# Kernel optimization log

Measured on AMD Instinct MI355X. Metric: run time of the kernel, lower is better.

The kernel has to match this reference:

```python
import jax, jax.numpy as jnp
import numpy as np

H = 128
EPS = 1e-5
INFERENCE_BIAS = 0.1


def setup_inputs() -> dict:
    key = jax.random.key(0)
    ks = jax.random.split(key, 10)
    n_users, n_foods, E = 100000, 50000, 1000000
    z_user = jax.random.normal(ks[0], (n_users, H), dtype=jnp.float32)
    z_food = jax.random.normal(ks[1], (n_foods, H), dtype=jnp.float32)
    row = jax.random.randint(ks[2], (E,), 0, n_users, dtype=jnp.int64)
    col = jax.random.randint(ks[3], (E,), 0, n_foods, dtype=jnp.int64)
    # lin1: Linear(2H -> H); lin2: Linear(H -> 1)
    W1 = jax.random.normal(ks[4], (H, 2 * H), dtype=jnp.float32) * (1.0 / np.sqrt(2 * H))
    b1 = jnp.zeros((H,), dtype=jnp.float32)
    gamma = jnp.ones((H,), dtype=jnp.float32)
    beta = jnp.zeros((H,), dtype=jnp.float32)
    running_mean = jax.random.normal(ks[5], (H,), dtype=jnp.float32) * 0.1
    running_var = jnp.abs(jax.random.normal(ks[6], (H,), dtype=jnp.float32)) * 0.1 + 1.0
    W2 = jax.random.normal(ks[7], (1, H), dtype=jnp.float32) * (1.0 / np.sqrt(H))
    b2 = jnp.zeros((1,), dtype=jnp.float32)
    return {"z_user": z_user, "z_food": z_food, "row": row, "col": col,
            "W1": W1, "b1": b1, "gamma": gamma, "beta": beta,
            "running_mean": running_mean, "running_var": running_var,
            "W2": W2, "b2": b2}


def reference(z_user, z_food, row, col, W1, b1, gamma, beta,
              running_mean, running_var, W2, b2):
    # gather per-edge endpoint embeddings and concat: [E, 2H]
    z = jnp.concatenate([z_user[row], z_food[col]], axis=-1)
    h = z @ W1.T + b1                                        # [E, H]
    # BatchNorm1d in eval mode: running statistics
    h = (h - running_mean) * jax.lax.rsqrt(running_var + EPS) * gamma + beta
    h = jax.nn.relu(h)                                        # dropout is identity in eval
    out = h @ W2.T + b2                                       # [E, 1]
    return jax.nn.sigmoid((out + INFERENCE_BIAS).reshape(-1)) # [E]
```

## Files before the change

### kernel.cpp

```cpp
#include <hip/hip_runtime.h>
#include <hip/hip_bf16.h>
#include <math.h>

#define H 128
#define EPS 1e-5f
#define INF_BIAS 0.1f

typedef __attribute__((ext_vector_type(8))) short bf16x8;
typedef __attribute__((ext_vector_type(4))) float f32x4;

__device__ inline unsigned short f2bf_rne(float f) {
    unsigned u = __float_as_uint(f);
    u += 0x7fffu + ((u >> 16) & 1u);
    return (unsigned short)(u >> 16);
}
__device__ inline float bf2f(unsigned short h) {
    return __uint_as_float(((unsigned)h) << 16);
}
__device__ inline unsigned pack2(float a, float b) {
    return (unsigned)f2bf_rne(a) | ((unsigned)f2bf_rne(b) << 16);
}
__device__ inline float2 unpack2(unsigned v) {
    float2 r;
    r.x = __uint_as_float(v << 16);
    r.y = __uint_as_float(v & 0xffff0000u);
    return r;
}

__global__ void prep_kernel(
    const float* __restrict__ W1, const float* __restrict__ b1,
    const float* __restrict__ gamma, const float* __restrict__ beta,
    const float* __restrict__ rm, const float* __restrict__ rv,
    unsigned short* __restrict__ Wswz_u, unsigned short* __restrict__ Wswz_f,
    float* __restrict__ d_user)
{
    const int f    = blockIdx.x;
    const int half = f >> 4, nt = (f >> 2) & 3, kt = f & 3;
    const int t    = threadIdx.x;
    const int c    = t & 15, q = t >> 4;

    const int j  = half * 64 + (c >> 2) * 16 + nt * 4 + (c & 3);
    const float a = gamma[j] * rsqrtf(rv[j] + EPS);
    const int k0 = kt * 32 + q * 8;

    unsigned short wu[8], wf[8];
    #pragma unroll
    for (int i = 0; i < 8; ++i) {
        wu[i] = f2bf_rne(a * W1[(size_t)j * (2 * H) + k0 + i]);
        wf[i] = f2bf_rne(a * W1[(size_t)j * (2 * H) + H + k0 + i]);
    }
    const size_t dst = (size_t)f * 512 + (size_t)t * 8;
    #pragma unroll
    for (int i = 0; i < 8; ++i) { Wswz_u[dst + i] = wu[i]; Wswz_f[dst + i] = wf[i]; }

    if (kt == 0 && q == 0) d_user[j] = a * (b1[j] - rm[j]) + beta[j];
}

__global__ __launch_bounds__(256, 2) void proj_mfma(
    const float* __restrict__ z_user, const float* __restrict__ z_food,
    const unsigned short* __restrict__ Wswz_u, const unsigned short* __restrict__ Wswz_f,
    const float* __restrict__ d_user,
    unsigned short* __restrict__ U, unsigned short* __restrict__ F,
    int n_users, int n_foods, int GU, int GB)
{
    const bool userMode = (blockIdx.x < (unsigned)GU);
    const float* Z;
    const unsigned short* Wsrc;
    unsigned short* Out;
    int n, blk0, nblk;
    if (userMode) { Z = z_user; Wsrc = Wswz_u; Out = U; n = n_users; blk0 = blockIdx.x;      nblk = GU; }
    else          { Z = z_food; Wsrc = Wswz_f; Out = F; n = n_foods; blk0 = blockIdx.x - GU; nblk = GB - GU; }
    const int tiles = n >> 4;

    const int wave = threadIdx.x >> 6;
    const int lane = threadIdx.x & 63;
    const int c = lane & 15;
    const int q = lane >> 4;
    const int wg   = blk0 * 4 + wave;
    const int half = wg & 1;
    const int pair = wg >> 1;
    const int stride = nblk * 2;

    bf16x8 wf[4][4];
    #pragma unroll
    for (int nt = 0; nt < 4; ++nt)
        #pragma unroll
        for (int kt = 0; kt < 4; ++kt)
            wf[nt][kt] = *(const bf16x8*)(Wsrc + (size_t)(half * 16 + nt * 4 + kt) * 512 + lane * 8);

    f32x4 dvec[4];
    #pragma unroll
    for (int nt = 0; nt < 4; ++nt) {
        if (userMode) {
            float4 d = *(const float4*)(d_user + half * 64 + q * 16 + nt * 4);
            dvec[nt] = (f32x4){d.x, d.y, d.z, d.w};
        } else {
            dvec[nt] = (f32x4){0.f, 0.f, 0.f, 0.f};
        }
    }

    auto loadZ = [&](int t, float4 zb[8]) {
        const float* zrow = Z + (size_t)(min(t, tiles - 1) * 16 + c) * H;
        #pragma unroll
        for (int kt = 0; kt < 4; ++kt) {
            const int k0 = kt * 32 + q * 8;
            zb[2 * kt + 0] = ((const float4*)(zrow + k0))[0];
            zb[2 * kt + 1] = ((const float4*)(zrow + k0))[1];
        }
    };

    auto computeStore = [&](int t, const float4 zb[8]) {
        f32x4 acc[4];
        #pragma unroll
        for (int nt = 0; nt < 4; ++nt) acc[nt] = dvec[nt];

        #pragma unroll
        for (int kt = 0; kt < 4; ++kt) {
            float4 za = zb[2 * kt + 0];
            float4 zv = zb[2 * kt + 1];
            bf16x8 zhi, zlo;
            {
                float v[8] = {za.x, za.y, za.z, za.w, zv.x, zv.y, zv.z, zv.w};
                #pragma unroll
                for (int i = 0; i < 8; ++i) {
                    unsigned short hi = f2bf_rne(v[i]);
                    unsigned short lo = f2bf_rne(v[i] - bf2f(hi));
                    zhi[i] = (short)hi; zlo[i] = (short)lo;
                }
            }
            #pragma unroll
            for (int nt = 0; nt < 4; ++nt) {
                acc[nt] = __builtin_amdgcn_mfma_f32_16x16x32_bf16(wf[nt][kt], zhi, acc[nt], 0, 0, 0);
                acc[nt] = __builtin_amdgcn_mfma_f32_16x16x32_bf16(wf[nt][kt], zlo, acc[nt], 0, 0, 0);
            }
        }

        if (t < tiles) {
            const int r = t * 16 + c;
            unsigned short* obase = Out + (size_t)r * H + half * 64 + q * 16;
            uint4 p0, p1;
            p0.x = pack2(acc[0][0], acc[0][1]); p0.y = pack2(acc[0][2], acc[0][3]);
            p0.z = pack2(acc[1][0], acc[1][1]); p0.w = pack2(acc[1][2], acc[1][3]);
            p1.x = pack2(acc[2][0], acc[2][1]); p1.y = pack2(acc[2][2], acc[2][3]);
            p1.z = pack2(acc[3][0], acc[3][1]); p1.w = pack2(acc[3][2], acc[3][3]);
            *(uint4*)(obase)     = p0;
            *(uint4*)(obase + 8) = p1;
        }
    };

    int nIt = (tiles + stride - 1) / stride;
    nIt = (nIt + 1) & ~1;

    float4 zb0[8], zb1[8];
    int t = pair;
    loadZ(t, zb0);
    for (int it = 0; it < nIt; it += 2) {
        loadZ(t + stride, zb1);
        computeStore(t, zb0);
        if (it + 2 < nIt) loadZ(t + 2 * stride, zb0);
        computeStore(t + stride, zb1);
        t += 2 * stride;
    }
}

#define EUN 8
__global__ __launch_bounds__(256, 4) void edge_kernel(
    const unsigned short* __restrict__ U, const unsigned short* __restrict__ F,
    const int* __restrict__ row, const int* __restrict__ col,
    const float* __restrict__ W2, const float* __restrict__ b2,
    float* __restrict__ out, int E)
{
    const int lane = threadIdx.x & 15;
    const int g  = (blockIdx.x * blockDim.x + threadIdx.x) >> 4;
    const int nG = (gridDim.x * blockDim.x) >> 4;

    const float4 w2a = ((const float4*)W2)[2 * lane];
    const float4 w2b = ((const float4*)W2)[2 * lane + 1];
    const float bias = b2[0] + INF_BIAS;

    for (int e0 = g; e0 < E; e0 += EUN * nG) {
        int iu[EUN], ifo[EUN];
        #pragma unroll
        for (int i = 0; i < EUN; ++i) {
            int e  = e0 + i * nG;
            int ec = (e < E) ? e : e0;
            iu[i]  = row[ec];
            ifo[i] = col[ec];
        }
        uint4 uv[EUN], fv[EUN];
        #pragma unroll
        for (int i = 0; i < EUN; ++i) {
            uv[i] = ((const uint4*)(U + (size_t)iu[i]  * H))[lane];
            fv[i] = ((const uint4*)(F + (size_t)ifo[i] * H))[lane];
        }
        #pragma unroll
        for (int i = 0; i < EUN; ++i) {
            float2 u0 = unpack2(uv[i].x), f0 = unpack2(fv[i].x);
            float2 u1 = unpack2(uv[i].y), f1 = unpack2(fv[i].y);
            float2 u2 = unpack2(uv[i].z), f2 = unpack2(fv[i].z);
            float2 u3 = unpack2(uv[i].w), f3 = unpack2(fv[i].w);

            float s =
                w2a.x * fmaxf(u0.x + f0.x, 0.0f) +
                w2a.y * fmaxf(u0.y + f0.y, 0.0f) +
                w2a.z * fmaxf(u1.x + f1.x, 0.0f) +
                w2a.w * fmaxf(u1.y + f1.y, 0.0f) +
                w2b.x * fmaxf(u2.x + f2.x, 0.0f) +
                w2b.y * fmaxf(u2.y + f2.y, 0.0f) +
                w2b.z * fmaxf(u3.x + f3.x, 0.0f) +
                w2b.w * fmaxf(u3.y + f3.y, 0.0f);

            s += __shfl_xor(s, 8, 16);
            s += __shfl_xor(s, 4, 16);
            s += __shfl_xor(s, 2, 16);
            s += __shfl_xor(s, 1, 16);

            const int e = e0 + i * nG;
            if (lane == 0 && e < E) {
                float x = s + bias;
                out[e] = 1.0f / (1.0f + __expf(-x));
            }
        }
    }
}

extern "C" void kernel_launch(void* const* d_in, const int* in_sizes, int n_in,
                              void* d_out, int out_size, void* d_ws, size_t ws_size,
                              hipStream_t stream) {
    const float* z_user = (const float*)d_in[0];
    const float* z_food = (const float*)d_in[1];
    const int*   row    = (const int*)d_in[2];
    const int*   col    = (const int*)d_in[3];
    const float* W1     = (const float*)d_in[4];
    const float* b1     = (const float*)d_in[5];
    const float* gamma  = (const float*)d_in[6];
    const float* beta   = (const float*)d_in[7];
    const float* rm     = (const float*)d_in[8];
    const float* rv     = (const float*)d_in[9];
    const float* W2     = (const float*)d_in[10];
    const float* b2     = (const float*)d_in[11];
    float* out = (float*)d_out;

    const int n_users = in_sizes[0] / H;
    const int n_foods = in_sizes[1] / H;
    const int E       = in_sizes[2];

    unsigned short* U      = (unsigned short*)d_ws;
    unsigned short* F      = U + (size_t)n_users * H;
    unsigned short* Wswz_u = F + (size_t)n_foods * H;
    unsigned short* Wswz_f = Wswz_u + H * H;
    float*          d_usr  = (float*)(Wswz_f + H * H);

    prep_kernel<<<32, 64, 0, stream>>>(W1, b1, gamma, beta, rm, rv,
                                       Wswz_u, Wswz_f, d_usr);

    const int GU = 342, GB = 512;
    proj_mfma<<<GB, 256, 0, stream>>>(z_user, z_food, Wswz_u, Wswz_f, d_usr,
                                      U, F, n_users, n_foods, GU, GB);

    edge_kernel<<<8192, 256, 0, stream>>>(U, F, row, col, W2, b2, out, E);
}
```

Baseline: 206.4 us.

## Stage projection weights in LDS and compute full 128-wide output per wave

```diff
diff --git a/kernel.cpp b/kernel.cpp
--- a/kernel.cpp
+++ b/kernel.cpp
@@ -63,6 +63,8 @@
     unsigned short* __restrict__ U, unsigned short* __restrict__ F,
     int n_users, int n_foods, int GU, int GB)
 {
+    __shared__ unsigned short Wlds[32 * 512];
+
     const bool userMode = (blockIdx.x < (unsigned)GU);
     const float* Z;
     const unsigned short* Wsrc;
@@ -72,30 +74,30 @@
     else          { Z = z_food; Wsrc = Wswz_f; Out = F; n = n_foods; blk0 = blockIdx.x - GU; nblk = GB - GU; }
     const int tiles = n >> 4;
 
+    {
+        const uint4* src = (const uint4*)Wsrc;
+        uint4* dst = (uint4*)Wlds;
+        #pragma unroll
+        for (int i = 0; i < 8; ++i)
+            dst[threadIdx.x + i * 256] = src[threadIdx.x + i * 256];
+    }
+    __syncthreads();
+
     const int wave = threadIdx.x >> 6;
     const int lane = threadIdx.x & 63;
     const int c = lane & 15;
     const int q = lane >> 4;
-    const int wg   = blk0 * 4 + wave;
-    const int half = wg & 1;
-    const int pair = wg >> 1;
-    const int stride = nblk * 2;
-
-    bf16x8 wf[4][4];
+    const int wg = blk0 * 4 + wave;
+    const int stride = nblk * 4;
+
+    f32x4 dvec[8];
     #pragma unroll
-    for (int nt = 0; nt < 4; ++nt)
-        #pragma unroll
-        for (int kt = 0; kt < 4; ++kt)
-            wf[nt][kt] = *(const bf16x8*)(Wsrc + (size_t)(half * 16 + nt * 4 + kt) * 512 + lane * 8);
-
-    f32x4 dvec[4];
-    #pragma unroll
-    for (int nt = 0; nt < 4; ++nt) {
+    for (int hn = 0; hn < 8; ++hn) {
         if (userMode) {
-            float4 d = *(const float4*)(d_user + half * 64 + q * 16 + nt * 4);
-            dvec[nt] = (f32x4){d.x, d.y, d.z, d.w};
+            float4 d = *(const float4*)(d_user + (hn >> 2) * 64 + q * 16 + (hn & 3) * 4);
+            dvec[hn] = (f32x4){d.x, d.y, d.z, d.w};
         } else {
-            dvec[nt] = (f32x4){0.f, 0.f, 0.f, 0.f};
+            dvec[hn] = (f32x4){0.f, 0.f, 0.f, 0.f};
         }
     }
 
@@ -110,9 +112,9 @@
     };
 
     auto computeStore = [&](int t, const float4 zb[8]) {
-        f32x4 acc[4];
-        #pragma unroll
-        for (int nt = 0; nt < 4; ++nt) acc[nt] = dvec[nt];
+        f32x4 acc[8];
+        #pragma unroll
+        for (int hn = 0; hn < 8; ++hn) acc[hn] = dvec[hn];
 
         #pragma unroll
         for (int kt = 0; kt < 4; ++kt) {
@@ -129,37 +131,48 @@
                 }
             }
             #pragma unroll
-            for (int nt = 0; nt < 4; ++nt) {
-                acc[nt] = __builtin_amdgcn_mfma_f32_16x16x32_bf16(wf[nt][kt], zhi, acc[nt], 0, 0, 0);
-                acc[nt] = __builtin_amdgcn_mfma_f32_16x16x32_bf16(wf[nt][kt], zlo, acc[nt], 0, 0, 0);
+            for (int hn = 0; hn < 8; ++hn) {
+                const int frag = (hn >> 2) * 16 + (hn & 3) * 4 + kt;
+                bf16x8 wfrag = *(const bf16x8*)(Wlds + (size_t)frag * 512 + lane * 8);
+                acc[hn] = __builtin_amdgcn_mfma_f32_16x16x32_bf16(wfrag, zhi, acc[hn], 0, 0, 0);
+                acc[hn] = __builtin_amdgcn_mfma_f32_16x16x32_bf16(wfrag, zlo, acc[hn], 0, 0, 0);
             }
         }
 
         if (t < tiles) {
             const int r = t * 16 + c;
-            unsigned short* obase = Out + (size_t)r * H + half * 64 + q * 16;
-            uint4 p0, p1;
+            unsigned short* obase = Out + (size_t)r * H + q * 16;
+            uint4 p0, p1, p2, p3;
             p0.x = pack2(acc[0][0], acc[0][1]); p0.y = pack2(acc[0][2], acc[0][3]);
             p0.z = pack2(acc[1][0], acc[1][1]); p0.w = pack2(acc[1][2], acc[1][3]);
             p1.x = pack2(acc[2][0], acc[2][1]); p1.y = pack2(acc[2][2], acc[2][3]);
             p1.z = pack2(acc[3][0], acc[3][1]); p1.w = pack2(acc[3][2], acc[3][3]);
-            *(uint4*)(obase)     = p0;
-            *(uint4*)(obase + 8) = p1;
+            p2.x = pack2(acc[4][0], acc[4][1]); p2.y = pack2(acc[4][2], acc[4][3]);
+            p2.z = pack2(acc[5][0], acc[5][1]); p2.w = pack2(acc[5][2], acc[5][3]);
+            p3.x = pack2(acc[6][0], acc[6][1]); p3.y = pack2(acc[6][2], acc[6][3]);
+            p3.z = pack2(acc[7][0], acc[7][1]); p3.w = pack2(acc[7][2], acc[7][3]);
+            *(uint4*)(obase)          = p0;
+            *(uint4*)(obase + 8)      = p1;
+            *(uint4*)(obase + 64)     = p2;
+            *(uint4*)(obase + 64 + 8) = p3;
         }
     };
 
     int nIt = (tiles + stride - 1) / stride;
-    nIt = (nIt + 1) & ~1;
-
-    float4 zb0[8], zb1[8];
-    int t = pair;
+    nIt = ((nIt + 2) / 3) * 3;
+
+    float4 zb0[8], zb1[8], zb2[8];
+    int t = wg;
     loadZ(t, zb0);
-    for (int it = 0; it < nIt; it += 2) {
-        loadZ(t + stride, zb1);
+    loadZ(t + stride, zb1);
+    for (int it = 0; it < nIt; it += 3) {
+        loadZ(t + 2 * stride, zb2);
         computeStore(t, zb0);
-        if (it + 2 < nIt) loadZ(t + 2 * stride, zb0);
+        loadZ(t + 3 * stride, zb0);
         computeStore(t + stride, zb1);
-        t += 2 * stride;
+        loadZ(t + 4 * stride, zb1);
+        computeStore(t + 2 * stride, zb2);
+        t += 3 * stride;
     }
 }
 
```

Result: slower. 215.9 us (+4.6%).
